# Performance work log

Measured on AMD Instinct MI355X. Metric: run time of the kernel, lower is better.

## Reference

```python
import jax, jax.numpy as jnp
import numpy as np

NUM_HEADS = 12
HEAD_SIZE = 64
HIDDEN = NUM_HEADS * HEAD_SIZE  # 768
ONE_SIDED_WINDOW = 256          # attention_window 512 // 2
NEG = -10000.0


def setup_inputs() -> dict:
    key = jax.random.key(0)
    ks = jax.random.split(key, 16)
    B, W, E, H = 1, 2048, 128, HIDDEN
    std = 0.02
    def lin(kw, kb):
        return (jax.random.normal(kw, (H, H), jnp.float32) * std,
                jax.random.normal(kb, (H,), jnp.float32) * std)
    q_w, q_b = lin(ks[0], ks[1])
    k_w, k_b = lin(ks[2], ks[3])
    v_w, v_b = lin(ks[4], ks[5])
    w2e_w, w2e_b = lin(ks[6], ks[7])
    e2w_w, e2w_b = lin(ks[8], ks[9])
    e2e_w, e2e_b = lin(ks[10], ks[11])
    return {
        "word_hidden_states": jax.random.normal(ks[12], (B, W, H), jnp.float32),
        "entity_hidden_states": jax.random.normal(ks[13], (B, E, H), jnp.float32),
        "attention_mask": jnp.zeros((B, 1, 1, W + E), jnp.float32),
        "q_w": q_w, "q_b": q_b, "k_w": k_w, "k_b": k_b, "v_w": v_w, "v_b": v_b,
        "w2e_w": w2e_w, "w2e_b": w2e_b, "e2w_w": e2w_w, "e2w_b": e2w_b,
        "e2e_w": e2e_w, "e2e_b": e2e_b,
    }


def reference(word_hidden_states, entity_hidden_states, attention_mask,
              q_w, q_b, k_w, k_b, v_w, v_b,
              w2e_w, w2e_b, e2w_w, e2w_b, e2e_w, e2e_b):
    B, W, H = word_hidden_states.shape
    E = entity_hidden_states.shape[1]
    S = W + E

    def heads(x):  # [B, L, H] -> [B, nh, L, hd]
        return x.reshape(B, -1, NUM_HEADS, HEAD_SIZE).transpose(0, 2, 1, 3)

    concat = jnp.concatenate([word_hidden_states, entity_hidden_states], axis=1)
    k = heads(concat @ k_w + k_b)          # [B, nh, S, hd]
    v = heads(concat @ v_w + v_b)
    q_w2w = heads(word_hidden_states @ q_w + q_b)
    q_w2e = heads(word_hidden_states @ w2e_w + w2e_b)
    q_e2w = heads(entity_hidden_states @ e2w_w + e2w_b)
    q_e2e = heads(entity_hidden_states @ e2e_w + e2e_b)

    k_word, k_ent = k[:, :, :W], k[:, :, W:]

    # --- w2w: Longformer sliding-window QK^T, then _conversion to a dense
    # [B, nh, W, W] matrix with out-of-band entries set to -10000. ---
    w2w = jnp.einsum('bhid,bhjd->bhij', q_w2w, k_word)  # [B, nh, W, W]
    idx = jnp.arange(W)
    in_band = jnp.abs(idx[:, None] - idx[None, :]) <= ONE_SIDED_WINDOW  # [W, W]
    # diagonal mask: float_mask[j] (-10000 where attention_mask != 0) added
    # within the band (broadcast over heads / query positions)
    mask_words = attention_mask[:, 0, 0, :W]                # [B, W]
    float_mask = jnp.where(mask_words != 0.0, NEG, 0.0)     # [B, W]
    w2w = w2w + float_mask[:, None, None, :]
    # _conversion: out-of-band -> -10000; also exact zeros -> -10000 (source quirk)
    w2w = jnp.where(in_band[None, None] & (w2w != 0.0), w2w, NEG)

    # --- entity-aware dense blocks ---
    w2e = jnp.einsum('bhid,bhjd->bhij', q_w2e, k_ent)    # [B, nh, W, E]
    e2w = jnp.einsum('bhid,bhjd->bhij', q_e2w, k_word)   # [B, nh, E, W]
    e2e = jnp.einsum('bhid,bhjd->bhij', q_e2e, k_ent)    # [B, nh, E, E]

    word_scores = jnp.concatenate([w2w, w2e], axis=3)    # [B, nh, W, S]
    ent_scores = jnp.concatenate([e2w, e2e], axis=3)     # [B, nh, E, S]
    scores = jnp.concatenate([word_scores, ent_scores], axis=2)  # [B, nh, S, S]

    scores = scores / jnp.sqrt(jnp.float32(HEAD_SIZE)) + attention_mask
    probs = jax.nn.softmax(scores, axis=-1)

    ctx = jnp.einsum('bhij,bhjd->bhid', probs, v)        # [B, nh, S, hd]
    ctx = ctx.transpose(0, 2, 1, 3).reshape(B, S, H)
    return ctx[:, :W, :], ctx[:, W:, :]
```

## Files before the change

### kernel.cpp

```cpp
#include <hip/hip_runtime.h>

typedef __bf16 bf16x8 __attribute__((ext_vector_type(8)));
typedef unsigned short u16x8 __attribute__((ext_vector_type(8)));
typedef u16x8 u16x8_a __attribute__((may_alias));
typedef unsigned short u16x4 __attribute__((ext_vector_type(4)));
typedef u16x4 u16x4_a __attribute__((may_alias));
typedef unsigned int u32x4 __attribute__((ext_vector_type(4)));
typedef u32x4 u32x4_a __attribute__((may_alias));
typedef float f32x4 __attribute__((ext_vector_type(4)));

#define LOG2E 1.4426950408889634f
#define NEGV  -10000.0f

__device__ __forceinline__ float bf2f(unsigned short u){
  union{unsigned int i; float f;} x; x.i = ((unsigned int)u)<<16; return x.f;
}
__device__ __forceinline__ unsigned short f2bf(float f){
  union{float f; unsigned int i;} x; x.f=f;
  unsigned int i = x.i;
  return (unsigned short)((i + 0x7FFFu + ((i>>16)&1u)) >> 16);
}
__device__ __forceinline__ bf16x8 ldb(const unsigned short* p){
  return __builtin_bit_cast(bf16x8, *(const u16x8_a*)p);
}

__global__ __launch_bounds__(256) void prep(
    const float* __restrict__ w0, const float* __restrict__ w1,
    const float* __restrict__ w2, const float* __restrict__ w3,
    const float* __restrict__ w4, const float* __restrict__ w5,
    const float* __restrict__ word, const float* __restrict__ ent,
    unsigned short* __restrict__ outT, unsigned short* __restrict__ Ab)
{
  int tx = threadIdx.x, ty = threadIdx.y;
  if (blockIdx.z == 6){
    int blk = blockIdx.y*24 + blockIdx.x;
    int gtid = blk*256 + ty*32 + tx;
    for (int idx = gtid; idx < 417792; idx += 147456){
      float4 v = (idx < 393216) ? ((const float4*)word)[idx]
                                : ((const float4*)ent)[idx - 393216];
      u16x4 r; r[0]=f2bf(v.x); r[1]=f2bf(v.y); r[2]=f2bf(v.z); r[3]=f2bf(v.w);
      *(u16x4_a*)(Ab + (size_t)idx*4) = r;
    }
    return;
  }
  const float* src;
  switch (blockIdx.z){
    case 0: src = w0; break; case 1: src = w1; break; case 2: src = w2; break;
    case 3: src = w3; break; case 4: src = w4; break; default: src = w5; break;
  }
  unsigned short* dst = outT + (size_t)blockIdx.z * 589824;
  __shared__ float tile[32][33];
  int x0 = blockIdx.x*32, y0 = blockIdx.y*32;
  #pragma unroll
  for (int i=0;i<32;i+=8) tile[ty+i][tx] = src[(size_t)(y0+ty+i)*768 + x0+tx];
  __syncthreads();
  #pragma unroll
  for (int i=0;i<32;i+=8) dst[(size_t)(x0+ty+i)*768 + y0+tx] = f2bf(tile[tx][ty+i]);
}

__global__ __launch_bounds__(256) void transpose_v(
    const unsigned short* __restrict__ Vb, unsigned short* __restrict__ VbT)
{
  __shared__ unsigned short t[32][33];
  int tx = threadIdx.x, ty = threadIdx.y;
  int x0 = blockIdx.x*32;
  int y0 = blockIdx.y*32;
  #pragma unroll
  for (int i=0;i<32;i+=8) t[ty+i][tx] = Vb[(size_t)(x0+ty+i)*768 + y0+tx];
  __syncthreads();
  #pragma unroll
  for (int i=0;i<32;i+=8) VbT[(size_t)(y0+ty+i)*2176 + x0+tx] = t[tx][ty+i];
}

__global__ __launch_bounds__(256) void gemm2(
    const unsigned short* __restrict__ Ab, const unsigned short* __restrict__ wT,
    const float* __restrict__ bK, const float* __restrict__ bV,
    const float* __restrict__ bQ, const float* __restrict__ bWE,
    const float* __restrict__ bEW, const float* __restrict__ bEE,
    unsigned short* __restrict__ oK, unsigned short* __restrict__ oV,
    unsigned short* __restrict__ oQ, unsigned short* __restrict__ oWE,
    unsigned short* __restrict__ oEW, unsigned short* __restrict__ oEE)
{
  int mt = blockIdx.x, ntile = blockIdx.y;
  int g, m0, mo;
  if      (mt < 34){ g=0; mo=mt;      m0=mo*64; }
  else if (mt < 68){ g=1; mo=mt-34;   m0=mo*64; }
  else if (mt <100){ g=2; mo=mt-68;   m0=mo*64; }
  else if (mt <132){ g=3; mo=mt-100;  m0=mo*64; }
  else if (mt <134){ g=4; mo=mt-132;  m0=2048+mo*64; }
  else             { g=5; mo=mt-134;  m0=2048+mo*64; }
  const unsigned short* A = Ab + (size_t)m0*768;
  const unsigned short* B = wT + (size_t)g*589824;
  const float* bias; unsigned short* out;
  switch (g){
    case 0: bias=bK;  out=oK  + (size_t)m0*768;    break;
    case 1: bias=bV;  out=oV  + (size_t)m0*768;    break;
    case 2: bias=bQ;  out=oQ  + (size_t)m0*768;    break;
    case 3: bias=bWE; out=oWE + (size_t)m0*768;    break;
    case 4: bias=bEW; out=oEW + (size_t)(mo*64)*768; break;
    default:bias=bEE; out=oEE + (size_t)(mo*64)*768; break;
  }
  int n0 = ntile*128;

  __shared__ __align__(16) unsigned short a_s[64*32];
  __shared__ __align__(16) unsigned short b_s[128*32];

  int tid  = threadIdx.x;
  int w    = tid>>6, lane = tid&63, quad = lane>>4, lr = lane&15;
  int wm   = (w&1)*32, wn = (w>>1)*64;

  f32x4 acc[2][4];
  #pragma unroll
  for (int i=0;i<2;i++) for (int j=0;j<4;j++) for (int r=0;r<4;r++) acc[i][j][r]=0.f;

  int ar = tid>>2, ak = (tid&3)*8;
  int br = tid>>1, bk = (tid&1)*16;
  const unsigned short* Arow = A + (size_t)ar*768 + ak;
  const unsigned short* Brow = B + (size_t)(n0+br)*768 + bk;

  for (int k0=0; k0<768; k0+=32){
    u16x8 av  = *(const u16x8_a*)(Arow + k0);
    u16x8 bv0 = *(const u16x8_a*)(Brow + k0);
    u16x8 bv1 = *(const u16x8_a*)(Brow + k0 + 8);
    __syncthreads();
    *(u16x8_a*)(a_s + ar*32 + ak)      = av;
    *(u16x8_a*)(b_s + br*32 + bk)      = bv0;
    *(u16x8_a*)(b_s + br*32 + bk + 8)  = bv1;
    __syncthreads();
    bf16x8 af[2], bfr[4];
    #pragma unroll
    for (int i=0;i<2;i++) af[i]  = ldb(a_s + (wm+i*16+lr)*32 + quad*8);
    #pragma unroll
    for (int j=0;j<4;j++) bfr[j] = ldb(b_s + (wn+j*16+lr)*32 + quad*8);
    #pragma unroll
    for (int i=0;i<2;i++)
      #pragma unroll
      for (int j=0;j<4;j++)
        acc[i][j] = __builtin_amdgcn_mfma_f32_16x16x32_bf16(af[i], bfr[j], acc[i][j], 0,0,0);
  }
  #pragma unroll
  for (int j=0;j<4;j++){
    int col = n0 + wn + j*16 + lr;
    float bb = bias[col];
    #pragma unroll
    for (int i=0;i<2;i++){
      int rowb = wm + i*16 + quad*4;
      #pragma unroll
      for (int r=0;r<4;r++)
        out[(size_t)(rowb+r)*768 + col] = f2bf(acc[i][j][r] + bb);
    }
  }
}

__global__ __launch_bounds__(256) void attn64(
  const unsigned short* __restrict__ Kb,  const unsigned short* __restrict__ VbT,
  const unsigned short* __restrict__ Qw,  const unsigned short* __restrict__ Qwe,
  const unsigned short* __restrict__ Qew, const unsigned short* __restrict__ Qee,
  const float* __restrict__ am,
  float* __restrict__ outw, float* __restrict__ oute)
{
  int id = blockIdx.x;
  int tid = threadIdx.x, w = tid>>6, lane = tid&63, quad = lane>>4, lr = lane&15;
  bool isword = id < 384;
  int h, qrb;
  const unsigned short *Qa, *Qb;
  float* outp;
  if (isword){
    int xcd = id & 7, pos = id >> 3;
    int wq  = (xcd<<2) | (pos & 3);
    h = pos >> 2;
    qrb = wq*64 + w*16;
    Qa = Qw; Qb = Qwe; outp = outw;
  } else {
    int eid = id - 384;
    h = eid % 12;
    qrb = (eid / 12) * 16;
    Qa = Qew; Qb = Qee; outp = oute;
  }

  __shared__ __align__(16) unsigned int p32[4][16*36];
  __shared__ float mrg[3][64][24];

  const unsigned short* qr = Qa + (size_t)(qrb+lr)*768 + h*64 + quad*8;
  bf16x8 qa0 = ldb(qr), qa1 = ldb(qr + 32);
  qr = Qb + (size_t)(qrb+lr)*768 + h*64 + quad*8;
  bf16x8 qb0 = ldb(qr), qb1 = ldb(qr + 32);

  float m_r[4], l_r[4];
  f32x4 o[4];
  #pragma unroll
  for (int r=0;r<4;r++){ m_r[r] = -1e30f; l_r[r] = 0.f; }
  #pragma unroll
  for (int n2=0;n2<4;n2++) for (int r=0;r<4;r++) o[n2][r] = 0.f;

  int lo, nw, cstart, cstep;
  if (isword){
    lo = qrb - 256; if (lo < 0) lo = 0; lo &= ~63;
    int hi = qrb + 272; if (hi > 2048) hi = 2048; hi = (hi + 63) & ~63;
    nw = (hi - lo) >> 6;
    cstart = 0; cstep = 1;
  } else { lo = 0; nw = 32; cstart = w; cstep = 4; }
  int nc = nw + 2;

  unsigned int* p32w = p32[w];

  for (int c = cstart; c < nc; c += cstep){
    bool entp = c >= nw;
    int j0 = entp ? (2048 + (c-nw)*64) : (lo + c*64);

    bf16x8 kf[4][2], vf[4][2];
    const unsigned short* kp = Kb + (size_t)(j0+lr)*768 + h*64 + quad*8;
    #pragma unroll
    for (int t=0;t<4;t++){
      kf[t][0] = ldb(kp + (size_t)t*16*768);
      kf[t][1] = ldb(kp + (size_t)t*16*768 + 32);
    }
    const unsigned short* vp = VbT + (size_t)(h*64 + lr)*2176 + j0 + quad*8;
    #pragma unroll
    for (int n2=0;n2<4;n2++){
      vf[n2][0] = ldb(vp + (size_t)n2*16*2176);
      vf[n2][1] = ldb(vp + (size_t)n2*16*2176 + 32);
    }

    bf16x8 qf0 = entp ? qb0 : qa0;
    bf16x8 qf1 = entp ? qb1 : qa1;
    f32x4 s[4];
    #pragma unroll
    for (int t=0;t<4;t++){
      f32x4 z = {0.f,0.f,0.f,0.f};
      z = __builtin_amdgcn_mfma_f32_16x16x32_bf16(qf0, kf[t][0], z, 0,0,0);
      z = __builtin_amdgcn_mfma_f32_16x16x32_bf16(qf1, kf[t][1], z, 0,0,0);
      s[t] = z;
    }

    float sc[4][4];
    bool wband = isword && !entp;
    #pragma unroll
    for (int t=0;t<4;t++){
      int j = j0 + t*16 + lr;
      float amj  = am[j];
      float addl = amj * LOG2E;
      #pragma unroll
      for (int r=0;r<4;r++){
        float sv = s[t][r];
        if (wband){
          sv += (amj != 0.f) ? NEGV : 0.f;
          int i = qrb + quad*4 + r;
          bool ok = ((unsigned)(i - j + 256) <= 512u) && (sv != 0.f);
          sv = ok ? sv : NEGV;
        }
        sc[t][r] = sv * (LOG2E*0.125f) + addl;
      }
    }

    #pragma unroll
    for (int r=0;r<4;r++){
      float mx = fmaxf(fmaxf(sc[0][r],sc[1][r]), fmaxf(sc[2][r],sc[3][r]));
      mx = fmaxf(mx, __shfl_xor(mx, 1));
      mx = fmaxf(mx, __shfl_xor(mx, 2));
      mx = fmaxf(mx, __shfl_xor(mx, 4));
      mx = fmaxf(mx, __shfl_xor(mx, 8));
      float mn = fmaxf(m_r[r], mx);
      float alpha = exp2f(m_r[r] - mn);
      m_r[r] = mn;
      float p0 = exp2f(sc[0][r]-mn), p1 = exp2f(sc[1][r]-mn);
      float p2 = exp2f(sc[2][r]-mn), p3 = exp2f(sc[3][r]-mn);
      unsigned short pb0 = f2bf(p0), pb1 = f2bf(p1);
      unsigned short pb2 = f2bf(p2), pb3 = f2bf(p3);
      float rs = (bf2f(pb0) + bf2f(pb1)) + (bf2f(pb2) + bf2f(pb3));
      rs += __shfl_xor(rs,1); rs += __shfl_xor(rs,2);
      rs += __shfl_xor(rs,4); rs += __shfl_xor(rs,8);
      l_r[r] = l_r[r]*alpha + rs;
      int row = quad*4 + r;
      p32w[row*36 + lr]      = (unsigned int)pb0 | ((unsigned int)pb1 << 16);
      p32w[row*36 + 16 + lr] = (unsigned int)pb2 | ((unsigned int)pb3 << 16);
      #pragma unroll
      for (int n2=0;n2<4;n2++) o[n2][r] *= alpha;
    }

    const unsigned int* pbp = &p32w[lr*36 + (quad&1)*8];
    u32x4 ra0 = *(const u32x4_a*)pbp;
    u32x4 rb0 = *(const u32x4_a*)(pbp + 4);
    u32x4 ra1 = *(const u32x4_a*)(pbp + 16);
    u32x4 rb1 = *(const u32x4_a*)(pbp + 20);
    unsigned int f0[4], f1[4];
    if (quad < 2){
      f0[0]=(ra0[0]&0xFFFFu)|(ra0[1]<<16); f0[1]=(ra0[2]&0xFFFFu)|(ra0[3]<<16);
      f0[2]=(rb0[0]&0xFFFFu)|(rb0[1]<<16); f0[3]=(rb0[2]&0xFFFFu)|(rb0[3]<<16);
      f1[0]=(ra1[0]&0xFFFFu)|(ra1[1]<<16); f1[1]=(ra1[2]&0xFFFFu)|(ra1[3]<<16);
      f1[2]=(rb1[0]&0xFFFFu)|(rb1[1]<<16); f1[3]=(rb1[2]&0xFFFFu)|(rb1[3]<<16);
    } else {
      f0[0]=(ra0[0]>>16)|(ra0[1]&0xFFFF0000u); f0[1]=(ra0[2]>>16)|(ra0[3]&0xFFFF0000u);
      f0[2]=(rb0[0]>>16)|(rb0[1]&0xFFFF0000u); f0[3]=(rb0[2]>>16)|(rb0[3]&0xFFFF0000u);
      f1[0]=(ra1[0]>>16)|(ra1[1]&0xFFFF0000u); f1[1]=(ra1[2]>>16)|(ra1[3]&0xFFFF0000u);
      f1[2]=(rb1[0]>>16)|(rb1[1]&0xFFFF0000u); f1[3]=(rb1[2]>>16)|(rb1[3]&0xFFFF0000u);
    }
    u32x4 v0v = {f0[0],f0[1],f0[2],f0[3]};
    u32x4 v1v = {f1[0],f1[1],f1[2],f1[3]};
    bf16x8 pf0 = __builtin_bit_cast(bf16x8, v0v);
    bf16x8 pf1 = __builtin_bit_cast(bf16x8, v1v);

    #pragma unroll
    for (int n2=0;n2<4;n2++){
      o[n2] = __builtin_amdgcn_mfma_f32_16x16x32_bf16(pf0, vf[n2][0], o[n2], 0,0,0);
      o[n2] = __builtin_amdgcn_mfma_f32_16x16x32_bf16(pf1, vf[n2][1], o[n2], 0,0,0);
    }
  }

  if (isword){
    #pragma unroll
    for (int n2=0;n2<4;n2++)
      #pragma unroll
      for (int r=0;r<4;r++){
        int row = qrb + quad*4 + r;
        outp[(size_t)row*768 + h*64 + n2*16 + lr] = o[n2][r] / l_r[r];
      }
  } else {
    if (w > 0){
      float* my = &mrg[w-1][lane][0];
      #pragma unroll
      for (int r=0;r<4;r++){ my[r] = m_r[r]; my[4+r] = l_r[r]; }
      #pragma unroll
      for (int n2=0;n2<4;n2++)
        #pragma unroll
        for (int r=0;r<4;r++) my[8+n2*4+r] = o[n2][r];
    }
    __syncthreads();
    if (w == 0){
      for (int p=0; p<3; p++){
        const float* pr = &mrg[p][lane][0];
        #pragma unroll
        for (int r=0;r<4;r++){
          float m2 = pr[r], l2 = pr[4+r];
          float M  = fmaxf(m_r[r], m2);
          float e1 = exp2f(m_r[r]-M), e2 = exp2f(m2-M);
          m_r[r] = M;
          l_r[r] = l_r[r]*e1 + l2*e2;
          #pragma unroll
          for (int n2=0;n2<4;n2++)
            o[n2][r] = o[n2][r]*e1 + pr[8+n2*4+r]*e2;
        }
      }
      #pragma unroll
      for (int n2=0;n2<4;n2++)
        #pragma unroll
        for (int r=0;r<4;r++){
          int row = qrb + quad*4 + r;
          outp[(size_t)row*768 + h*64 + n2*16 + lr] = o[n2][r] / l_r[r];
        }
    }
  }
}

extern "C" void kernel_launch(void* const* d_in, const int* in_sizes, int n_in,
                              void* d_out, int out_size, void* d_ws, size_t ws_size,
                              hipStream_t stream) {
  const float* word  = (const float*)d_in[0];
  const float* ent   = (const float*)d_in[1];
  const float* am    = (const float*)d_in[2];
  const float* q_w   = (const float*)d_in[3];
  const float* q_b   = (const float*)d_in[4];
  const float* k_w   = (const float*)d_in[5];
  const float* k_b   = (const float*)d_in[6];
  const float* v_w   = (const float*)d_in[7];
  const float* v_b   = (const float*)d_in[8];
  const float* w2e_w = (const float*)d_in[9];
  const float* w2e_b = (const float*)d_in[10];
  const float* e2w_w = (const float*)d_in[11];
  const float* e2w_b = (const float*)d_in[12];
  const float* e2e_w = (const float*)d_in[13];
  const float* e2e_b = (const float*)d_in[14];

  unsigned short* ws  = (unsigned short*)d_ws;
  unsigned short* wT  = ws;
  unsigned short* Ab  = wT  + (size_t)6*589824;
  unsigned short* Kb  = Ab  + (size_t)2176*768;
  unsigned short* Vb  = Kb  + (size_t)2176*768;
  unsigned short* Qw  = Vb  + (size_t)2176*768;
  unsigned short* Qwe = Qw  + (size_t)2048*768;
  unsigned short* Qew = Qwe + (size_t)2048*768;
  unsigned short* Qee = Qew + (size_t)128*768;
  unsigned short* VbT = Qee + (size_t)128*768;

  float* outw = (float*)d_out;
  float* oute = outw + (size_t)2048*768;

  hipLaunchKernelGGL(prep, dim3(24,24,7), dim3(32,8), 0, stream,
                     k_w, v_w, q_w, w2e_w, e2w_w, e2e_w, word, ent, wT, Ab);
  hipLaunchKernelGGL(gemm2, dim3(136,6), dim3(256), 0, stream,
                     Ab, wT, k_b, v_b, q_b, w2e_b, e2w_b, e2e_b,
                     Kb, Vb, Qw, Qwe, Qew, Qee);
  hipLaunchKernelGGL(transpose_v, dim3(68,24), dim3(32,8), 0, stream, Vb, VbT);
  hipLaunchKernelGGL(attn64, dim3(480), dim3(256), 0, stream,
                     Kb, VbT, Qw, Qwe, Qew, Qee, am, outw, oute);
}
```

Baseline: 184.7 us.

## Fuse V transpose into GEMM epilogue and split word attention keys across warps

The projection GEMM now writes V directly in transposed layout from its epilogue, which removes the separate transpose kernel and one round trip of V through global memory. The attention kernel assigns each 16-row word query block to its own workgroup. The four warps stride over key chunks, and their partial softmax states are merged through shared memory in a two-level tree, so the grid grows from 480 to 1632 blocks. This raises parallelism for the sliding-window part. In exchange, each block reloads the Q fragments, adds merge barriers, and makes 8-byte strided stores for V^T.

```diff
diff --git a/kernel.cpp b/kernel.cpp
--- a/kernel.cpp
+++ b/kernel.cpp
@@ -58,26 +58,12 @@
   for (int i=0;i<32;i+=8) dst[(size_t)(x0+ty+i)*768 + y0+tx] = f2bf(tile[tx][ty+i]);
 }
 
-__global__ __launch_bounds__(256) void transpose_v(
-    const unsigned short* __restrict__ Vb, unsigned short* __restrict__ VbT)
-{
-  __shared__ unsigned short t[32][33];
-  int tx = threadIdx.x, ty = threadIdx.y;
-  int x0 = blockIdx.x*32;
-  int y0 = blockIdx.y*32;
-  #pragma unroll
-  for (int i=0;i<32;i+=8) t[ty+i][tx] = Vb[(size_t)(x0+ty+i)*768 + y0+tx];
-  __syncthreads();
-  #pragma unroll
-  for (int i=0;i<32;i+=8) VbT[(size_t)(y0+ty+i)*2176 + x0+tx] = t[tx][ty+i];
-}
-
 __global__ __launch_bounds__(256) void gemm2(
     const unsigned short* __restrict__ Ab, const unsigned short* __restrict__ wT,
     const float* __restrict__ bK, const float* __restrict__ bV,
     const float* __restrict__ bQ, const float* __restrict__ bWE,
     const float* __restrict__ bEW, const float* __restrict__ bEE,
-    unsigned short* __restrict__ oK, unsigned short* __restrict__ oV,
+    unsigned short* __restrict__ oK, unsigned short* __restrict__ oVT,
     unsigned short* __restrict__ oQ, unsigned short* __restrict__ oWE,
     unsigned short* __restrict__ oEW, unsigned short* __restrict__ oEE)
 {
@@ -94,7 +80,7 @@
   const float* bias; unsigned short* out;
   switch (g){
     case 0: bias=bK;  out=oK  + (size_t)m0*768;    break;
-    case 1: bias=bV;  out=oV  + (size_t)m0*768;    break;
+    case 1: bias=bV;  out=0;                        break;
     case 2: bias=bQ;  out=oQ  + (size_t)m0*768;    break;
     case 3: bias=bWE; out=oWE + (size_t)m0*768;    break;
     case 4: bias=bEW; out=oEW + (size_t)(mo*64)*768; break;
@@ -138,21 +124,37 @@
       for (int j=0;j<4;j++)
         acc[i][j] = __builtin_amdgcn_mfma_f32_16x16x32_bf16(af[i], bfr[j], acc[i][j], 0,0,0);
   }
-  #pragma unroll
-  for (int j=0;j<4;j++){
-    int col = n0 + wn + j*16 + lr;
-    float bb = bias[col];
-    #pragma unroll
-    for (int i=0;i<2;i++){
-      int rowb = wm + i*16 + quad*4;
-      #pragma unroll
-      for (int r=0;r<4;r++)
-        out[(size_t)(rowb+r)*768 + col] = f2bf(acc[i][j][r] + bb);
-    }
-  }
-}
-
-__global__ __launch_bounds__(256) void attn64(
+  if (g == 1){
+    #pragma unroll
+    for (int j=0;j<4;j++){
+      int col = n0 + wn + j*16 + lr;
+      float bb = bias[col];
+      #pragma unroll
+      for (int i=0;i<2;i++){
+        int key0 = m0 + wm + i*16 + quad*4;
+        u16x4 pk;
+        #pragma unroll
+        for (int r=0;r<4;r++) pk[r] = f2bf(acc[i][j][r] + bb);
+        *(u16x4_a*)(oVT + (size_t)col*2176 + key0) = pk;
+      }
+    }
+  } else {
+    #pragma unroll
+    for (int j=0;j<4;j++){
+      int col = n0 + wn + j*16 + lr;
+      float bb = bias[col];
+      #pragma unroll
+      for (int i=0;i<2;i++){
+        int rowb = wm + i*16 + quad*4;
+        #pragma unroll
+        for (int r=0;r<4;r++)
+          out[(size_t)(rowb+r)*768 + col] = f2bf(acc[i][j][r] + bb);
+      }
+    }
+  }
+}
+
+__global__ __launch_bounds__(256) void attn64s(
   const unsigned short* __restrict__ Kb,  const unsigned short* __restrict__ VbT,
   const unsigned short* __restrict__ Qw,  const unsigned short* __restrict__ Qwe,
   const unsigned short* __restrict__ Qew, const unsigned short* __restrict__ Qee,
@@ -161,25 +163,25 @@
 {
   int id = blockIdx.x;
   int tid = threadIdx.x, w = tid>>6, lane = tid&63, quad = lane>>4, lr = lane&15;
-  bool isword = id < 384;
+  bool isword = id < 1536;
   int h, qrb;
   const unsigned short *Qa, *Qb;
   float* outp;
   if (isword){
     int xcd = id & 7, pos = id >> 3;
-    int wq  = (xcd<<2) | (pos & 3);
-    h = pos >> 2;
-    qrb = wq*64 + w*16;
+    h = pos >> 4;
+    int lc = pos & 15;
+    qrb = (xcd*16 + lc) * 16;
     Qa = Qw; Qb = Qwe; outp = outw;
   } else {
-    int eid = id - 384;
+    int eid = id - 1536;
     h = eid % 12;
     qrb = (eid / 12) * 16;
     Qa = Qew; Qb = Qee; outp = oute;
   }
 
   __shared__ __align__(16) unsigned int p32[4][16*36];
-  __shared__ float mrg[3][64][24];
+  __shared__ float mrg[2][64][24];
 
   const unsigned short* qr = Qa + (size_t)(qrb+lr)*768 + h*64 + quad*8;
   bf16x8 qa0 = ldb(qr), qa1 = ldb(qr + 32);
@@ -193,18 +195,17 @@
   #pragma unroll
   for (int n2=0;n2<4;n2++) for (int r=0;r<4;r++) o[n2][r] = 0.f;
 
-  int lo, nw, cstart, cstep;
+  int lo, nw;
   if (isword){
     lo = qrb - 256; if (lo < 0) lo = 0; lo &= ~63;
     int hi = qrb + 272; if (hi > 2048) hi = 2048; hi = (hi + 63) & ~63;
     nw = (hi - lo) >> 6;
-    cstart = 0; cstep = 1;
-  } else { lo = 0; nw = 32; cstart = w; cstep = 4; }
+  } else { lo = 0; nw = 32; }
   int nc = nw + 2;
 
   unsigned int* p32w = p32[w];
 
-  for (int c = cstart; c < nc; c += cstep){
+  for (int c = w; c < nc; c += 4){
     bool entp = c >= nw;
     int j0 = entp ? (2048 + (c-nw)*64) : (lo + c*64);
 
@@ -307,7 +308,54 @@
     }
   }
 
-  if (isword){
+  if (w == 1 || w == 3){
+    float* my = &mrg[w>>1][lane][0];
+    #pragma unroll
+    for (int r=0;r<4;r++){ my[r] = m_r[r]; my[4+r] = l_r[r]; }
+    #pragma unroll
+    for (int n2=0;n2<4;n2++)
+      #pragma unroll
+      for (int r=0;r<4;r++) my[8+n2*4+r] = o[n2][r];
+  }
+  __syncthreads();
+  if (w == 0 || w == 2){
+    const float* pr = &mrg[w>>1][lane][0];
+    #pragma unroll
+    for (int r=0;r<4;r++){
+      float m2 = pr[r], l2 = pr[4+r];
+      float M  = fmaxf(m_r[r], m2);
+      float e1 = exp2f(m_r[r]-M), e2 = exp2f(m2-M);
+      m_r[r] = M;
+      l_r[r] = l_r[r]*e1 + l2*e2;
+      #pragma unroll
+      for (int n2=0;n2<4;n2++)
+        o[n2][r] = o[n2][r]*e1 + pr[8+n2*4+r]*e2;
+    }
+  }
+  __syncthreads();
+  if (w == 2){
+    float* my = &mrg[0][lane][0];
+    #pragma unroll
+    for (int r=0;r<4;r++){ my[r] = m_r[r]; my[4+r] = l_r[r]; }
+    #pragma unroll
+    for (int n2=0;n2<4;n2++)
+      #pragma unroll
+      for (int r=0;r<4;r++) my[8+n2*4+r] = o[n2][r];
+  }
+  __syncthreads();
+  if (w == 0){
+    const float* pr = &mrg[0][lane][0];
+    #pragma unroll
+    for (int r=0;r<4;r++){
+      float m2 = pr[r], l2 = pr[4+r];
+      float M  = fmaxf(m_r[r], m2);
+      float e1 = exp2f(m_r[r]-M), e2 = exp2f(m2-M);
+      m_r[r] = M;
+      l_r[r] = l_r[r]*e1 + l2*e2;
+      #pragma unroll
+      for (int n2=0;n2<4;n2++)
+        o[n2][r] = o[n2][r]*e1 + pr[8+n2*4+r]*e2;
+    }
     #pragma unroll
     for (int n2=0;n2<4;n2++)
       #pragma unroll
@@ -315,40 +363,6 @@
         int row = qrb + quad*4 + r;
         outp[(size_t)row*768 + h*64 + n2*16 + lr] = o[n2][r] / l_r[r];
       }
-  } else {
-    if (w > 0){
-      float* my = &mrg[w-1][lane][0];
-      #pragma unroll
-      for (int r=0;r<4;r++){ my[r] = m_r[r]; my[4+r] = l_r[r]; }
-      #pragma unroll
-      for (int n2=0;n2<4;n2++)
-        #pragma unroll
-        for (int r=0;r<4;r++) my[8+n2*4+r] = o[n2][r];
-    }
-    __syncthreads();
-    if (w == 0){
-      for (int p=0; p<3; p++){
-        const float* pr = &mrg[p][lane][0];
-        #pragma unroll
-        for (int r=0;r<4;r++){
-          float m2 = pr[r], l2 = pr[4+r];
-          float M  = fmaxf(m_r[r], m2);
-          float e1 = exp2f(m_r[r]-M), e2 = exp2f(m2-M);
-          m_r[r] = M;
-          l_r[r] = l_r[r]*e1 + l2*e2;
-          #pragma unroll
-          for (int n2=0;n2<4;n2++)
-            o[n2][r] = o[n2][r]*e1 + pr[8+n2*4+r]*e2;
-        }
-      }
-      #pragma unroll
-      for (int n2=0;n2<4;n2++)
-        #pragma unroll
-        for (int r=0;r<4;r++){
-          int row = qrb + quad*4 + r;
-          outp[(size_t)row*768 + h*64 + n2*16 + lr] = o[n2][r] / l_r[r];
-        }
-    }
   }
 }
 
@@ -375,12 +389,11 @@
   unsigned short* wT  = ws;
   unsigned short* Ab  = wT  + (size_t)6*589824;
   unsigned short* Kb  = Ab  + (size_t)2176*768;
-  unsigned short* Vb  = Kb  + (size_t)2176*768;
-  unsigned short* Qw  = Vb  + (size_t)2176*768;
+  unsigned short* VbT = Kb  + (size_t)2176*768;
+  unsigned short* Qw  = VbT + (size_t)768*2176;
   unsigned short* Qwe = Qw  + (size_t)2048*768;
   unsigned short* Qew = Qwe + (size_t)2048*768;
   unsigned short* Qee = Qew + (size_t)128*768;
-  unsigned short* VbT = Qee + (size_t)128*768;
 
   float* outw = (float*)d_out;
   float* oute = outw + (size_t)2048*768;
@@ -389,8 +402,7 @@
                      k_w, v_w, q_w, w2e_w, e2w_w, e2e_w, word, ent, wT, Ab);
   hipLaunchKernelGGL(gemm2, dim3(136,6), dim3(256), 0, stream,
                      Ab, wT, k_b, v_b, q_b, w2e_b, e2w_b, e2e_b,
-                     Kb, Vb, Qw, Qwe, Qew, Qee);
-  hipLaunchKernelGGL(transpose_v, dim3(68,24), dim3(32,8), 0, stream, Vb, VbT);
-  hipLaunchKernelGGL(attn64, dim3(480), dim3(256), 0, stream,
+                     Kb, VbT, Qw, Qwe, Qew, Qee);
+  hipLaunchKernelGGL(attn64s, dim3(1632), dim3(256), 0, stream,
                      Kb, VbT, Qw, Qwe, Qew, Qee, am, outw, oute);
 }
```

Result: slower. 201.4 us (+9.1%).
